# Kernel optimization log

Hardware: AMD Instinct MI355X
Metric: run time of the kernel (lower is better)

Reference implementation:

```python
import jax, jax.numpy as jnp
import numpy as np

S = 9                      # spiral length
V = [8192, 4096, 2048, 1024, 512]  # verts per level, finest -> latent


def grid_sample_bilinear(feat, grid):
    # feat [B,C,H,W], grid [B,P,2] in [-1,1]; bilinear, align_corners=True
    B, C, H, W = feat.shape
    x = (grid[..., 0] + 1.0) * 0.5 * (W - 1)
    y = (grid[..., 1] + 1.0) * 0.5 * (H - 1)
    x0 = jnp.floor(x); y0 = jnp.floor(y)
    wx = x - x0; wy = y - y0
    x0i = jnp.clip(x0.astype(jnp.int32), 0, W - 1)
    x1i = jnp.clip(x0.astype(jnp.int32) + 1, 0, W - 1)
    y0i = jnp.clip(y0.astype(jnp.int32), 0, H - 1)
    y1i = jnp.clip(y0.astype(jnp.int32) + 1, 0, H - 1)
    featf = feat.reshape(B, C, H * W).transpose(0, 2, 1)  # [B,HW,C]
    def gat(yi, xi):
        return jnp.take_along_axis(featf, (yi * W + xi)[..., None], axis=1)  # [B,P,C]
    w00 = ((1 - wy) * (1 - wx))[..., None]
    w01 = ((1 - wy) * wx)[..., None]
    w10 = (wy * (1 - wx))[..., None]
    w11 = (wy * wx)[..., None]
    return gat(y0i, x0i) * w00 + gat(y0i, x1i) * w01 + gat(y1i, x0i) * w10 + gat(y1i, x1i) * w11


def pool(x, row, col, val):
    # sparse mesh upsample: gather cols, scale, scatter-add into rows
    n_out = row.shape[0] // 3
    g = x[:, col, :] * val[None, :, None]                       # [B,nnz,C]
    return jnp.zeros((x.shape[0], n_out, x.shape[-1]), x.dtype).at[:, row, :].add(g)


def dsconv(x, idx, wd, wp, b):
    # depthwise-separable spiral conv: gather spiral ring, depthwise over S, pointwise mix
    g = x[:, idx]                                # [B,N,S,C]
    dw = jnp.einsum('bnsc,sc->bnc', g, wd)       # depthwise over spiral dim
    return jnp.einsum('bnc,co->bno', dw, wp) + b # pointwise


def _forward(uv, feat, upsample, s0, s1, s2, s3,
             row0, col0, val0, row1, col1, val1, row2, col2, val2, row3, col3, val3,
             wd0, wp0, b0, wd1, wp1, b1, wd2, wp2, b2, wd3, wp3, b3, wdh, wph, bh):
    uvc = jnp.clip((uv - 0.5) * 2.0, -1.0, 1.0)
    x = grid_sample_bilinear(feat, uvc)           # [B,P,C]  (torch: [B,C,P] then permute)
    x = jnp.einsum('vp,bpc->bvc', upsample, x)    # [B,V4,C] latent mesh features
    x = jax.nn.relu(dsconv(pool(x, row3, col3, val3), s3, wd0, wp0, b0))  # [B,1024,512]
    x = jax.nn.relu(dsconv(pool(x, row2, col2, val2), s2, wd1, wp1, b1))  # [B,2048,256]
    x = jax.nn.relu(dsconv(pool(x, row1, col1, val1), s1, wd2, wp2, b2))  # [B,4096,128]
    x = jax.nn.relu(dsconv(pool(x, row0, col0, val0), s0, wd3, wp3, b3))  # [B,8192,64]
    return dsconv(x, s0, wdh, wph, bh)            # [B,8192,3]


def setup_inputs():
    ks = jax.random.split(jax.random.key(0), 64)
    B, P, C, H, W = 8, 21, 512, 32, 32
    inp = {}
    inp['uv'] = jax.random.uniform(ks[0], (B, P, 2), jnp.float32)
    inp['feat'] = jax.random.normal(ks[1], (B, C, H, W), jnp.float32)
    inp['upsample'] = 0.01 * jnp.ones((V[4], P), jnp.float32)
    for i in range(4):
        inp[f's{i}'] = jax.random.randint(ks[2 + i], (V[i], S), 0, V[i])
    for i in range(4):
        nnz = 3 * V[i]
        inp[f'row{i}'] = jax.random.randint(ks[6 + 3 * i], (nnz,), 0, V[i])
        inp[f'col{i}'] = jax.random.randint(ks[7 + 3 * i], (nnz,), 0, V[i + 1])
        inp[f'val{i}'] = jax.random.uniform(ks[8 + 3 * i], (nnz,), jnp.float32)
    chans = [(512, 512), (512, 256), (256, 128), (128, 64), (64, 3)]
    names = ['0', '1', '2', '3', 'h']
    k = 20
    for (ci, co), nm in zip(chans, names):
        inp[f'wd{nm}'] = 0.1 * jax.random.normal(ks[k], (S, ci), jnp.float32); k += 1
        inp[f'wp{nm}'] = jax.random.normal(ks[k], (ci, co), jnp.float32) * (1.0 / float(np.sqrt(ci))); k += 1
        inp[f'b{nm}'] = jnp.zeros((co,), jnp.float32); k += 1
    return inp


def reference(uv, feat, upsample, s0, s1, s2, s3,
              row0, col0, val0, row1, col1, val1, row2, col2, val2, row3, col3, val3,
              wd0, wp0, b0, wd1, wp1, b1, wd2, wp2, b2, wd3, wp3, b3, wdh, wph, bh):
    return _forward(uv, feat, upsample, s0, s1, s2, s3,
                    row0, col0, val0, row1, col1, val1, row2, col2, val2, row3, col3, val3,
                    wd0, wp0, b0, wd1, wp1, b1, wd2, wp2, b2, wd3, wp3, b3, wdh, wph, bh)
```

## Files before the change

### kernel.cpp

```cpp
#include <hip/hip_runtime.h>

#define B_  8
#define P_  21
#define H_  32
#define W_  32

typedef float f32x4 __attribute__((ext_vector_type(4)));
typedef _Float16 f16x8 __attribute__((ext_vector_type(8)));

struct CsrParams {
  const int*   row[4];
  const int*   col[4];
  const float* val[4];
  int*   rowptr[4];
  int*   colsout[4];
  float* valsout[4];
  int    nnz[4];
  int    V[4];
};

__global__ __launch_bounds__(1024) void csr_build_kernel(CsrParams p) {
  __shared__ int cnt[8192];
  __shared__ int partial[1024];
  const int l   = blockIdx.x;
  const int V   = p.V[l];
  const int nnz = p.nnz[l];
  const int t   = threadIdx.x;
  const int* row = p.row[l];

  for (int i = t; i < V; i += 1024) cnt[i] = 0;
  __syncthreads();
  for (int k = t; k < nnz; k += 1024) atomicAdd(&cnt[row[k]], 1);
  __syncthreads();

  const int chunk = V >> 10;
  const int base  = t * chunk;
  int s = 0;
  for (int i = 0; i < chunk; ++i) s += cnt[base + i];
  partial[t] = s;
  __syncthreads();
  for (int off = 1; off < 1024; off <<= 1) {
    int v = (t >= off) ? partial[t - off] : 0;
    __syncthreads();
    partial[t] += v;
    __syncthreads();
  }
  int run = partial[t] - s;
  int* rp = p.rowptr[l];
  for (int i = 0; i < chunk; ++i) {
    int c = cnt[base + i];
    rp[base + i]  = run;
    cnt[base + i] = run;
    run += c;
  }
  if (t == 1023) rp[V] = nnz;
  __syncthreads();

  const int*   col = p.col[l];
  const float* val = p.val[l];
  int*   co = p.colsout[l];
  float* va = p.valsout[l];
  for (int k = t; k < nnz; k += 1024) {
    int r = row[k];
    int pos = atomicAdd(&cnt[r], 1);
    co[pos] = col[k];
    va[pos] = val[k];
  }
}

__global__ void sample_kernel(const float* __restrict__ uv,
                              const float* __restrict__ feat,
                              float* __restrict__ xs) {
  int bp = blockIdx.x;
  int b  = bp / P_;
  float u0 = uv[bp * 2 + 0], u1 = uv[bp * 2 + 1];
  float gx = fminf(fmaxf((u0 - 0.5f) * 2.0f, -1.0f), 1.0f);
  float gy = fminf(fmaxf((u1 - 0.5f) * 2.0f, -1.0f), 1.0f);
  float fx = (gx + 1.0f) * 0.5f * (W_ - 1);
  float fy = (gy + 1.0f) * 0.5f * (H_ - 1);
  float x0f = floorf(fx), y0f = floorf(fy);
  float wx = fx - x0f, wy = fy - y0f;
  int x0 = (int)x0f, y0 = (int)y0f;
  int x0i = min(max(x0, 0), W_ - 1), x1i = min(max(x0 + 1, 0), W_ - 1);
  int y0i = min(max(y0, 0), H_ - 1), y1i = min(max(y0 + 1, 0), H_ - 1);
  float w00 = (1.f - wy) * (1.f - wx), w01 = (1.f - wy) * wx;
  float w10 = wy * (1.f - wx),        w11 = wy * wx;
  for (int c = threadIdx.x; c < 512; c += blockDim.x) {
    const float* fb = feat + ((size_t)(b * 512 + c)) * (H_ * W_);
    float v = fb[y0i * W_ + x0i] * w00 + fb[y0i * W_ + x1i] * w01 +
              fb[y1i * W_ + x0i] * w10 + fb[y1i * W_ + x1i] * w11;
    xs[(size_t)bp * 512 + c] = v;
  }
}

__global__ void upsample_kernel(const float* __restrict__ up,
                                const float* __restrict__ xs,
                                float* __restrict__ xu) {
  int v = blockIdx.x, b = blockIdx.y;
  int c4 = threadIdx.x << 2;
  float4 acc = make_float4(0.f, 0.f, 0.f, 0.f);
  for (int p = 0; p < P_; ++p) {
    float u = up[v * P_ + p];
    const float4 xv = *(const float4*)&xs[((size_t)(b * P_ + p)) * 512 + c4];
    acc.x = fmaf(u, xv.x, acc.x);
    acc.y = fmaf(u, xv.y, acc.y);
    acc.z = fmaf(u, xv.z, acc.z);
    acc.w = fmaf(u, xv.w, acc.w);
  }
  *(float4*)&xu[((size_t)(b * 512 + v)) * 512 + c4] = acc;
}

__global__ __launch_bounds__(256) void pool_kernel(
    const float* __restrict__ x,
    const int* __restrict__ rowptr,
    const int* __restrict__ cols,
    const float* __restrict__ vals,
    float* __restrict__ out,
    int Vout, int Vin, int Cin) {
  const int lpr    = Cin >> 3;
  const int lshift = 31 - __clz(lpr);
  const int rpb    = 256 >> lshift;
  const int lr = threadIdx.x >> lshift;
  const int lc = threadIdx.x & (lpr - 1);
  const int b  = blockIdx.x & 7;
  const int n  = (blockIdx.x >> 3) * rpb + lr;
  const int c8 = lc << 3;
  const float* xb = x + (size_t)b * Vin * Cin + c8;
  int j0 = rowptr[n], j1 = rowptr[n + 1];
  float4 a0 = make_float4(0.f, 0.f, 0.f, 0.f);
  float4 a1 = make_float4(0.f, 0.f, 0.f, 0.f);
  for (int j = j0; j < j1; ++j) {
    float v = vals[j];
    const float* xr = xb + (size_t)cols[j] * Cin;
    float4 x0 = *(const float4*)xr;
    float4 x1 = *(const float4*)(xr + 4);
    a0.x = fmaf(v, x0.x, a0.x); a0.y = fmaf(v, x0.y, a0.y);
    a0.z = fmaf(v, x0.z, a0.z); a0.w = fmaf(v, x0.w, a0.w);
    a1.x = fmaf(v, x1.x, a1.x); a1.y = fmaf(v, x1.y, a1.y);
    a1.z = fmaf(v, x1.z, a1.z); a1.w = fmaf(v, x1.w, a1.w);
  }
  float* op = &out[((size_t)b * Vout + n) * Cin + c8];
  *(float4*)op = a0;
  *(float4*)(op + 4) = a1;
}

__global__ __launch_bounds__(256) void dw_split_kernel(
    const float* __restrict__ xin,
    const int* __restrict__ sidx,
    const float* __restrict__ wd,
    _Float16* __restrict__ a0o,
    _Float16* __restrict__ a1o,
    int Vout, int Cin) {
  const int lpr    = Cin >> 3;
  const int lshift = 31 - __clz(lpr);
  const int rpb    = 256 >> lshift;
  const int lr = threadIdx.x >> lshift;
  const int lc = threadIdx.x & (lpr - 1);
  const int b  = blockIdx.x & 7;
  const int n  = (blockIdx.x >> 3) * rpb + lr;
  const int c8 = lc << 3;
  const float* xb = xin + (size_t)b * Vout * Cin + c8;

  int idx[9];
  #pragma unroll
  for (int s = 0; s < 9; ++s) idx[s] = sidx[n * 9 + s];

  float4 a0 = make_float4(0.f, 0.f, 0.f, 0.f);
  float4 a1 = make_float4(0.f, 0.f, 0.f, 0.f);
  #pragma unroll
  for (int s = 0; s < 9; ++s) {
    const float* xr = xb + (size_t)idx[s] * Cin;
    float4 x0 = *(const float4*)xr;
    float4 x1 = *(const float4*)(xr + 4);
    const float* wr = wd + s * Cin + c8;
    float4 w0 = *(const float4*)wr;
    float4 w1 = *(const float4*)(wr + 4);
    a0.x = fmaf(w0.x, x0.x, a0.x); a0.y = fmaf(w0.y, x0.y, a0.y);
    a0.z = fmaf(w0.z, x0.z, a0.z); a0.w = fmaf(w0.w, x0.w, a0.w);
    a1.x = fmaf(w1.x, x1.x, a1.x); a1.y = fmaf(w1.y, x1.y, a1.y);
    a1.z = fmaf(w1.z, x1.z, a1.z); a1.w = fmaf(w1.w, x1.w, a1.w);
  }

  size_t m = (size_t)b * Vout + n;
  float v[8] = {a0.x, a0.y, a0.z, a0.w, a1.x, a1.y, a1.z, a1.w};
  f16x8 hi, lo;
  #pragma unroll
  for (int i = 0; i < 8; ++i) {
    _Float16 h0 = (_Float16)v[i];
    float r = (v[i] - (float)h0) * 2048.0f;
    hi[i] = h0;
    lo[i] = (_Float16)r;
  }
  *(f16x8*)&a0o[m * Cin + c8] = hi;
  *(f16x8*)&a1o[m * Cin + c8] = lo;
}

struct BsplitParams {
  const float* wp[4];
  int K[4], N[4], off[4];
  _Float16* b0;
  _Float16* b1;
};

__global__ void bsplit_all_kernel(BsplitParams p) {
  int idx = blockIdx.x * 256 + threadIdx.x;
  #pragma unroll
  for (int t = 0; t < 4; ++t) {
    int sz = p.N[t] * p.K[t];
    if (idx < sz) {
      int n = idx / p.K[t], k = idx - n * p.K[t];
      float v = p.wp[t][(size_t)k * p.N[t] + n];
      _Float16 h0 = (_Float16)v;
      float r = (v - (float)h0) * 2048.0f;
      p.b0[p.off[t] + idx] = h0;
      p.b1[p.off[t] + idx] = (_Float16)r;
      return;
    }
    idx -= sz;
  }
}

__global__ __launch_bounds__(256) void gemm_f16x2(
    const _Float16* __restrict__ A0, const _Float16* __restrict__ A1,
    const _Float16* __restrict__ Bt0, const _Float16* __restrict__ Bt1,
    const float* __restrict__ bias, float* __restrict__ C,
    int M, int N, int K) {
  constexpr int RP = 72;
  __shared__ _Float16 As[2][128][RP];
  __shared__ _Float16 Bs[2][64][RP];
  const int tid = threadIdx.x;
  const int bx = blockIdx.x;
  const int xr_ = (bx & 7) * (gridDim.x >> 3) + (bx >> 3);
  const int m0 = xr_ * 128, n0 = blockIdx.y * 64;
  const int wid = tid >> 6, lane = tid & 63;
  const int wr = wid >> 1, wc = wid & 1;
  const int lo = lane & 15, hi = lane >> 4;

  f32x4 accM[4][2], accC[4][2];
  #pragma unroll
  for (int mi = 0; mi < 4; ++mi)
    #pragma unroll
    for (int nj = 0; nj < 2; ++nj) {
      accM[mi][nj] = (f32x4){0.f, 0.f, 0.f, 0.f};
      accC[mi][nj] = (f32x4){0.f, 0.f, 0.f, 0.f};
    }

  const _Float16* gA[2] = {A0, A1};
  const _Float16* gB[2] = {Bt0, Bt1};

  for (int k0 = 0; k0 < K; k0 += 64) {
    #pragma unroll
    for (int p = 0; p < 2; ++p) {
      #pragma unroll
      for (int i = 0; i < 4; ++i) {
        int c = tid + 256 * i;
        int r = c >> 3, k8 = (c & 7) << 3;
        uint4 v = *(const uint4*)(gA[p] + (size_t)(m0 + r) * K + k0 + k8);
        *(uint4*)&As[p][r][k8] = v;
      }
      #pragma unroll
      for (int i = 0; i < 2; ++i) {
        int c = tid + 256 * i;
        int r = c >> 3, k8 = (c & 7) << 3;
        uint4 v = *(const uint4*)(gB[p] + (size_t)(n0 + r) * K + k0 + k8);
        *(uint4*)&Bs[p][r][k8] = v;
      }
    }
    __syncthreads();
    #pragma unroll
    for (int s = 0; s < 2; ++s) {
      const int kk = s * 32 + hi * 8;
      f16x8 af[4][2], bf[2][2];
      #pragma unroll
      for (int mi = 0; mi < 4; ++mi) {
        af[mi][0] = *(const f16x8*)&As[0][wr * 64 + mi * 16 + lo][kk];
        af[mi][1] = *(const f16x8*)&As[1][wr * 64 + mi * 16 + lo][kk];
      }
      #pragma unroll
      for (int nj = 0; nj < 2; ++nj) {
        bf[nj][0] = *(const f16x8*)&Bs[0][wc * 32 + nj * 16 + lo][kk];
        bf[nj][1] = *(const f16x8*)&Bs[1][wc * 32 + nj * 16 + lo][kk];
      }
      #pragma unroll
      for (int mi = 0; mi < 4; ++mi)
        #pragma unroll
        for (int nj = 0; nj < 2; ++nj) {
          accM[mi][nj] = __builtin_amdgcn_mfma_f32_16x16x32_f16(
              af[mi][0], bf[nj][0], accM[mi][nj], 0, 0, 0);
          accC[mi][nj] = __builtin_amdgcn_mfma_f32_16x16x32_f16(
              af[mi][0], bf[nj][1], accC[mi][nj], 0, 0, 0);
          accC[mi][nj] = __builtin_amdgcn_mfma_f32_16x16x32_f16(
              af[mi][1], bf[nj][0], accC[mi][nj], 0, 0, 0);
        }
    }
    __syncthreads();
  }

  const float INV = 1.0f / 2048.0f;
  #pragma unroll
  for (int mi = 0; mi < 4; ++mi)
    #pragma unroll
    for (int nj = 0; nj < 2; ++nj) {
      int col = n0 + wc * 32 + nj * 16 + lo;
      float bv = bias[col];
      #pragma unroll
      for (int r = 0; r < 4; ++r) {
        int row = m0 + wr * 64 + mi * 16 + hi * 4 + r;
        float v = accM[mi][nj][r] + accC[mi][nj][r] * INV + bv;
        v = fmaxf(v, 0.f);
        C[(size_t)row * N + col] = v;
      }
    }
}

__global__ __launch_bounds__(256) void head_fused_kernel(
    const float* __restrict__ x,
    const int* __restrict__ sidx,
    const float* __restrict__ wdh,
    const float* __restrict__ wph,
    const float* __restrict__ bh,
    float* __restrict__ out) {
  const int bid  = blockIdx.x;
  const int b    = bid & 7;
  const int wid  = threadIdx.x >> 6;
  const int lane = threadIdx.x & 63;
  const int n    = (bid >> 3) * 4 + wid;
  const float* xb = x + (size_t)b * 8192 * 64 + lane;

  int idx[9];
  #pragma unroll
  for (int s = 0; s < 9; ++s) idx[s] = sidx[n * 9 + s];

  float acc = 0.f;
  #pragma unroll
  for (int s = 0; s < 9; ++s)
    acc = fmaf(wdh[s * 64 + lane], xb[(size_t)idx[s] * 64], acc);

  float a0 = acc * wph[lane * 3 + 0];
  float a1 = acc * wph[lane * 3 + 1];
  float a2 = acc * wph[lane * 3 + 2];
  for (int off = 32; off > 0; off >>= 1) {
    a0 += __shfl_down(a0, off);
    a1 += __shfl_down(a1, off);
    a2 += __shfl_down(a2, off);
  }
  if (lane == 0) {
    size_t row = (size_t)b * 8192 + n;
    out[row * 3 + 0] = a0 + bh[0];
    out[row * 3 + 1] = a1 + bh[1];
    out[row * 3 + 2] = a2 + bh[2];
  }
}

extern "C" void kernel_launch(void* const* d_in, const int* in_sizes, int n_in,
                              void* d_out, int out_size, void* d_ws, size_t ws_size,
                              hipStream_t stream) {
  const float* uv   = (const float*)d_in[0];
  const float* feat = (const float*)d_in[1];
  const float* up   = (const float*)d_in[2];
  const int* sArr[4] = {(const int*)d_in[3], (const int*)d_in[4],
                        (const int*)d_in[5], (const int*)d_in[6]};

  const size_t SLAB = 8ull * 2048 * 512;
  float* Wf = (float*)d_ws;
  float* S0 = Wf;
  float* S1 = Wf + SLAB;
  _Float16* A0 = (_Float16*)(S1 + SLAB);
  _Float16* A1 = A0 + SLAB;
  _Float16* Bt0all = (_Float16*)(S0 + 4500000);
  _Float16* Bt1all = Bt0all + 434176;
  float* xs = (float*)(A1 + SLAB);
  int* ib = (int*)(xs + (size_t)B_ * P_ * 512);

  int Vt[4] = {1024, 2048, 4096, 8192};
  int NZ[4] = {3072, 6144, 12288, 24576};
  int* rp[4]; int* co[4]; float* va[4];
  {
    int* pc = ib;
    for (int t = 0; t < 4; ++t) { rp[t] = pc; pc += Vt[t] + 1; }
    for (int t = 0; t < 4; ++t) { co[t] = pc; pc += NZ[t]; }
    float* pv = (float*)pc;
    for (int t = 0; t < 4; ++t) { va[t] = pv; pv += NZ[t]; }
  }

  CsrParams cp;
  for (int t = 0; t < 4; ++t) {
    int i = 3 - t;
    cp.row[t] = (const int*)d_in[7 + 3 * i];
    cp.col[t] = (const int*)d_in[8 + 3 * i];
    cp.val[t] = (const float*)d_in[9 + 3 * i];
    cp.rowptr[t] = rp[t];
    cp.colsout[t] = co[t]; cp.valsout[t] = va[t];
    cp.nnz[t] = NZ[t]; cp.V[t] = Vt[t];
  }

  csr_build_kernel<<<4, 1024, 0, stream>>>(cp);
  sample_kernel<<<B_ * P_, 256, 0, stream>>>(uv, feat, xs);
  upsample_kernel<<<dim3(512, B_), 128, 0, stream>>>(up, xs, S0);

  struct Stg { int Vin, Vout, Cin, Cout; const int* s; const float *wd, *wp, *bias; };
  Stg st[4] = {
    {512, 1024, 512, 512, sArr[3], (const float*)d_in[19], (const float*)d_in[20], (const float*)d_in[21]},
    {1024, 2048, 512, 256, sArr[2], (const float*)d_in[22], (const float*)d_in[23], (const float*)d_in[24]},
    {2048, 4096, 256, 128, sArr[1], (const float*)d_in[25], (const float*)d_in[26], (const float*)d_in[27]},
    {4096, 8192, 128, 64, sArr[0], (const float*)d_in[28], (const float*)d_in[29], (const float*)d_in[30]},
  };

  BsplitParams bp;
  int boff = 0;
  for (int t = 0; t < 4; ++t) {
    bp.wp[t] = st[t].wp;
    bp.K[t] = st[t].Cin; bp.N[t] = st[t].Cout;
    bp.off[t] = boff;
    boff += st[t].Cin * st[t].Cout;
  }
  bp.b0 = Bt0all; bp.b1 = Bt1all;
  bsplit_all_kernel<<<(boff + 255) / 256, 256, 0, stream>>>(bp);

  for (int t = 0; t < 4; ++t) {
    int rpb = 2048 / st[t].Cin;
    pool_kernel<<<8 * (st[t].Vout / rpb), 256, 0, stream>>>(
        S0, rp[t], co[t], va[t], S1, st[t].Vout, st[t].Vin, st[t].Cin);
    dw_split_kernel<<<8 * (st[t].Vout / rpb), 256, 0, stream>>>(
        S1, st[t].s, st[t].wd, A0, A1, st[t].Vout, st[t].Cin);
    int M = B_ * st[t].Vout;
    gemm_f16x2<<<dim3(M / 128, st[t].Cout / 64), 256, 0, stream>>>(
        A0, A1, Bt0all + bp.off[t], Bt1all + bp.off[t],
        st[t].bias, S0, M, st[t].Cout, st[t].Cin);
  }

  head_fused_kernel<<<8 * (8192 / 4), 256, 0, stream>>>(
      S0, sArr[0], (const float*)d_in[31], (const float*)d_in[32],
      (const float*)d_in[33], (float*)d_out);
}
```

Before: 298.9 us.

## Split single-block CSR build into parallel count, scan and fill kernels

The four-block CSR build, which ran one 1024-thread block per level with shared-memory atomics, is replaced by a memset, a multi-block count kernel using global atomics, a small scan kernel and a multi-block fill kernel. The aim is to spread the histogram and scatter work across many CUs instead of four. The cost is three extra launches plus a memset, and atomics that now go to global memory. Row order within each row still depends on atomic ordering, as it did before.

After: 280.1 us. -6.3%, faster.

```diff
diff --git a/kernel.cpp b/kernel.cpp
--- a/kernel.cpp
+++ b/kernel.cpp
@@ -12,6 +12,7 @@
   const int*   row[4];
   const int*   col[4];
   const float* val[4];
+  int*   cnt[4];
   int*   rowptr[4];
   int*   colsout[4];
   float* valsout[4];
@@ -19,52 +20,49 @@
   int    V[4];
 };
 
-__global__ __launch_bounds__(1024) void csr_build_kernel(CsrParams p) {
-  __shared__ int cnt[8192];
-  __shared__ int partial[1024];
-  const int l   = blockIdx.x;
-  const int V   = p.V[l];
-  const int nnz = p.nnz[l];
-  const int t   = threadIdx.x;
-  const int* row = p.row[l];
-
-  for (int i = t; i < V; i += 1024) cnt[i] = 0;
-  __syncthreads();
-  for (int k = t; k < nnz; k += 1024) atomicAdd(&cnt[row[k]], 1);
-  __syncthreads();
-
-  const int chunk = V >> 10;
-  const int base  = t * chunk;
+__global__ void count_kernel(CsrParams p) {
+  int l = blockIdx.y;
+  int k = blockIdx.x * 256 + threadIdx.x;
+  if (k < p.nnz[l]) atomicAdd(&p.cnt[l][p.row[l][k]], 1);
+}
+
+__global__ void scan_kernel(CsrParams p) {
+  int l = blockIdx.x;
+  int V = p.V[l];
+  int* cnt = p.cnt[l];
+  int* rp  = p.rowptr[l];
+  int t = threadIdx.x;
+  int chunk = V / 256;
+  int base = t * chunk;
   int s = 0;
   for (int i = 0; i < chunk; ++i) s += cnt[base + i];
-  partial[t] = s;
+  __shared__ int sm[256];
+  sm[t] = s;
   __syncthreads();
-  for (int off = 1; off < 1024; off <<= 1) {
-    int v = (t >= off) ? partial[t - off] : 0;
+  for (int off = 1; off < 256; off <<= 1) {
+    int v = (t >= off) ? sm[t - off] : 0;
     __syncthreads();
-    partial[t] += v;
+    sm[t] += v;
     __syncthreads();
   }
-  int run = partial[t] - s;
-  int* rp = p.rowptr[l];
+  int run = sm[t] - s;
   for (int i = 0; i < chunk; ++i) {
     int c = cnt[base + i];
     rp[base + i]  = run;
     cnt[base + i] = run;
     run += c;
   }
-  if (t == 1023) rp[V] = nnz;
-  __syncthreads();
-
-  const int*   col = p.col[l];
-  const float* val = p.val[l];
-  int*   co = p.colsout[l];
-  float* va = p.valsout[l];
-  for (int k = t; k < nnz; k += 1024) {
-    int r = row[k];
-    int pos = atomicAdd(&cnt[r], 1);
-    co[pos] = col[k];
-    va[pos] = val[k];
+  if (t == 255) rp[V] = run;
+}
+
+__global__ void fill_kernel(CsrParams p) {
+  int l = blockIdx.y;
+  int k = blockIdx.x * 256 + threadIdx.x;
+  if (k < p.nnz[l]) {
+    int r = p.row[l][k];
+    int pos = atomicAdd(&p.cnt[l][r], 1);
+    p.colsout[l][pos] = p.col[l][k];
+    p.valsout[l][pos] = p.val[l][k];
   }
 }
 
@@ -374,9 +372,10 @@
 
   int Vt[4] = {1024, 2048, 4096, 8192};
   int NZ[4] = {3072, 6144, 12288, 24576};
-  int* rp[4]; int* co[4]; float* va[4];
+  int* cnt[4]; int* rp[4]; int* co[4]; float* va[4];
   {
     int* pc = ib;
+    for (int t = 0; t < 4; ++t) { cnt[t] = pc; pc += Vt[t]; }
     for (int t = 0; t < 4; ++t) { rp[t] = pc; pc += Vt[t] + 1; }
     for (int t = 0; t < 4; ++t) { co[t] = pc; pc += NZ[t]; }
     float* pv = (float*)pc;
@@ -389,12 +388,16 @@
     cp.row[t] = (const int*)d_in[7 + 3 * i];
     cp.col[t] = (const int*)d_in[8 + 3 * i];
     cp.val[t] = (const float*)d_in[9 + 3 * i];
-    cp.rowptr[t] = rp[t];
+    cp.cnt[t] = cnt[t]; cp.rowptr[t] = rp[t];
     cp.colsout[t] = co[t]; cp.valsout[t] = va[t];
     cp.nnz[t] = NZ[t]; cp.V[t] = Vt[t];
   }
 
-  csr_build_kernel<<<4, 1024, 0, stream>>>(cp);
+  hipMemsetAsync(ib, 0, 15360 * sizeof(int), stream);
+  count_kernel<<<dim3(96, 4), 256, 0, stream>>>(cp);
+  scan_kernel<<<4, 256, 0, stream>>>(cp);
+  fill_kernel<<<dim3(96, 4), 256, 0, stream>>>(cp);
+
   sample_kernel<<<B_ * P_, 256, 0, stream>>>(uv, feat, xs);
   upsample_kernel<<<dim3(512, B_), 128, 0, stream>>>(up, xs, S0);
 
```
